# Performance work log

Measured on AMD Instinct MI355X. Metric: run time of the kernel, lower is better.

Reference implementation:

```python
import jax, jax.numpy as jnp
import numpy as np

D = 2048
B = 32768
EPS = 1e-5


def _branch_params(key, d):
    k1, k2 = jax.random.split(key)
    s1 = 1.0 / np.sqrt(d)
    return dict(
        W1=jax.random.uniform(k1, (d, d), jnp.float32, -s1, s1),
        b1=jnp.zeros((d,), jnp.float32),
        ln_g=jnp.ones((d,), jnp.float32),
        ln_b=jnp.zeros((d,), jnp.float32),
        W2=jax.random.uniform(k2, (2, d), jnp.float32, -s1, s1),
        b2=jnp.zeros((2,), jnp.float32),
    )


def setup_inputs() -> dict:
    key = jax.random.key(0)
    kx, kf, ka, kr = jax.random.split(key, 4)
    x = jax.random.normal(kx, (B, D), jnp.float32)
    inp = {"x": x}
    for name, k in (("first", kf), ("fake", ka), ("real", kr)):
        p = _branch_params(k, D)
        for pn, pv in p.items():
            inp[f"{name}_{pn}"] = pv
    return inp


def _branch(x, W1, b1, g, be, W2, b2):
    # Linear(d,d) -> LayerNorm(d) -> ReLU -> Linear(d,2); Dropout is identity at eval.
    h = x @ W1.T + b1                                   # [B, D]
    mu = jnp.mean(h, axis=-1, keepdims=True)
    var = jnp.mean(jnp.square(h - mu), axis=-1, keepdims=True)
    h = (h - mu) * jax.lax.rsqrt(var + EPS) * g + be
    h = jax.nn.relu(h)
    return h @ W2.T + b2                                # [B, 2]


def reference(x,
              first_W1, first_b1, first_ln_g, first_ln_b, first_W2, first_b2,
              fake_W1, fake_b1, fake_ln_g, fake_ln_b, fake_W2, fake_b2,
              real_W1, real_b1, real_ln_g, real_ln_b, real_W2, real_b2):
    first_logits = _branch(x, first_W1, first_b1, first_ln_g, first_ln_b, first_W2, first_b2)
    route = jnp.argmax(first_logits, axis=1)            # [B], 0 -> fake expert, else real
    fake_logits = _branch(x, fake_W1, fake_b1, fake_ln_g, fake_ln_b, fake_W2, fake_b2)
    real_logits = _branch(x, real_W1, real_b1, real_ln_g, real_ln_b, real_W2, real_b2)
    final_logits = jnp.where((route == 0)[:, None], fake_logits, real_logits)  # [B, 2]
    return final_logits
```

## Files before the change

### kernel.cpp

```cpp
#include <hip/hip_runtime.h>

#define BD 32768
#define DD 2048
#define LN_EPS 1e-5f
#define MARGIN 0.03f
#define UCAP 8192
#define IDX_CAP 33280

typedef unsigned short u16;
typedef unsigned int u32;
typedef __bf16 bf16x8 __attribute__((ext_vector_type(8)));
typedef float floatx4 __attribute__((ext_vector_type(4)));

__device__ inline u16 f2bf(float f) {
    u32 u = __builtin_bit_cast(u32, f);
    u32 r = (u + 0x7fffu + ((u >> 16) & 1u)) >> 16;
    return (u16)r;
}
__device__ inline float bf2f(u16 h) {
    return __builtin_bit_cast(float, ((u32)h) << 16);
}
__device__ inline void bf2x2(u32 p, float& lo, float& hi) {
    lo = __builtin_bit_cast(float, p << 16);
    hi = __builtin_bit_cast(float, p & 0xffff0000u);
}

__device__ inline void lds16(const void* g, void* l) {
    __builtin_amdgcn_global_load_lds(
        (const __attribute__((address_space(1))) u32*)g,
        (__attribute__((address_space(3))) u32*)l, 16, 0, 0);
}

__global__ __launch_bounds__(256) void zero_misc(int* idx_all, int* u_idx, int* ctrl) {
    int t = blockIdx.x * 256 + threadIdx.x;
    if (t < IDX_CAP) idx_all[t] = 0;
    if (t < UCAP) u_idx[t] = 0;
    if (t < 8) ctrl[t] = 0;
}

__global__ __launch_bounds__(256) void split_xhi(const float* __restrict__ in,
                                                 u16* __restrict__ hi, int n4) {
    int i = blockIdx.x * 256 + threadIdx.x;
    if (i >= n4) return;
    float4 f = ((const float4*)in)[i];
    ((ushort4*)hi)[i] = make_ushort4(f2bf(f.x), f2bf(f.y), f2bf(f.z), f2bf(f.w));
}

__global__ __launch_bounds__(256) void split_xlo(const float* __restrict__ x,
                                                 const int* __restrict__ u_idx,
                                                 const int* __restrict__ ctrl,
                                                 u16* __restrict__ xlo) {
    int u = ctrl[1]; if (u > UCAP) u = UCAP;
    int r = blockIdx.x;
    if (r >= u) return;
    int orig = u_idx[r];
    const float4* src = (const float4*)(x + (size_t)orig * DD);
    ushort4* dst = (ushort4*)(xlo + (size_t)r * DD);
    int i = threadIdx.x;
#pragma unroll
    for (int k = 0; k < 2; ++k, i += 256) {
        float4 f = src[i];
        u16 h0 = f2bf(f.x), h1 = f2bf(f.y), h2 = f2bf(f.z), h3 = f2bf(f.w);
        dst[i] = make_ushort4(f2bf(f.x - bf2f(h0)), f2bf(f.y - bf2f(h1)),
                              f2bf(f.z - bf2f(h2)), f2bf(f.w - bf2f(h3)));
    }
}

__global__ __launch_bounds__(256) void split_w3(const float* __restrict__ w0,
                                                const float* __restrict__ w1,
                                                const float* __restrict__ w2,
                                                u16* h0, u16* l0p,
                                                u16* h1, u16* l1p,
                                                u16* h2, u16* l2p) {
    int i = blockIdx.x * 256 + threadIdx.x;
    int m = blockIdx.y;
    const float* in = (m == 0) ? w0 : (m == 1) ? w1 : w2;
    u16* hi = (m == 0) ? h0 : (m == 1) ? h1 : h2;
    u16* lo = (m == 0) ? l0p : (m == 1) ? l1p : l2p;
    float4 f = ((const float4*)in)[i];
    u16 a0 = f2bf(f.x), a1 = f2bf(f.y), a2 = f2bf(f.z), a3 = f2bf(f.w);
    u16 b0 = f2bf(f.x - bf2f(a0)), b1 = f2bf(f.y - bf2f(a1));
    u16 b2 = f2bf(f.z - bf2f(a2)), b3 = f2bf(f.w - bf2f(a3));
    ((ushort4*)hi)[i] = make_ushort4(a0, a1, a2, a3);
    ((ushort4*)lo)[i] = make_ushort4(b0, b1, b2, b3);
}

template <int IDX, int DUAL>
__global__ __launch_bounds__(512, 2) void gemm256(const u16* __restrict__ A,
                                                  const u16* __restrict__ B1,
                                                  const u16* __restrict__ B2,
                                                  u16* __restrict__ C,
                                                  const int* __restrict__ ridx,
                                                  const int* __restrict__ ctrl) {
    const int nwg = (int)(gridDim.x * gridDim.y);
    const int wg0 = (int)(blockIdx.y * gridDim.x + blockIdx.x);
    const int chunk = nwg >> 3;
    const int swz = (wg0 & 7) * chunk + (wg0 >> 3);
    const size_t bm = (size_t)(swz >> 3) * 256;
    const size_t bn = (size_t)(swz & 7) * 256;

    const u16* Bp = B1;
    if (DUAL) {
        int nf_pad = ctrl[3];
        int limit = nf_pad + (BD - ctrl[2]);
        if ((int)bm >= limit) return;
        if ((int)bm >= nf_pad) Bp = B2;
    }

    __shared__ alignas(16) u16 smem[65536];
    const int tid = threadIdx.x;
    const int lane = tid & 63;
    const int wave = tid >> 6;
    const int wr = wave >> 2, wc = wave & 3;
    const int m16 = lane & 15, q4 = lane >> 4;

    const int srow = tid >> 3;
    const int kq = ((tid & 7) ^ (srow & 7)) * 8;
    const int tid8 = tid * 8;
    size_t aOff[4], bOff[4];
#pragma unroll
    for (int s = 0; s < 4; ++s) {
        int row = s * 64 + srow;
        int g = IDX ? ridx[bm + row] : (int)(bm + row);
        aOff[s] = (size_t)g * DD + kq;
        bOff[s] = (size_t)(bn + row) * DD + kq;
    }

    const int slot0 = ((q4) ^ (m16 & 7)) * 8;
    const int slot1 = ((4 + q4) ^ (m16 & 7)) * 8;
    const int aFr = (wr * 128 + m16) * 64;
    const int bFr = 16384 + (wc * 64 + m16) * 64;

    floatx4 acc[8][4] = {};

#define STAGE_TILE(DB, K0)                                              \
    lds16(A + aOff[0] + (K0), &smem[(DB) + 0 * 4096 + tid8]);           \
    lds16(A + aOff[1] + (K0), &smem[(DB) + 1 * 4096 + tid8]);           \
    lds16(A + aOff[2] + (K0), &smem[(DB) + 2 * 4096 + tid8]);           \
    lds16(A + aOff[3] + (K0), &smem[(DB) + 3 * 4096 + tid8]);           \
    lds16(Bp + bOff[0] + (K0), &smem[(DB) + 16384 + 0 * 4096 + tid8]);  \
    lds16(Bp + bOff[1] + (K0), &smem[(DB) + 16384 + 1 * 4096 + tid8]);  \
    lds16(Bp + bOff[2] + (K0), &smem[(DB) + 16384 + 2 * 4096 + tid8]);  \
    lds16(Bp + bOff[3] + (K0), &smem[(DB) + 16384 + 3 * 4096 + tid8]);

    STAGE_TILE(0, 0)

    int base = 0;
    const int NT = DD / 64;
    for (int t = 0; t < NT; ++t) {
        const int nbase = base ^ 32768;
        __builtin_amdgcn_s_barrier();
        if (t + 1 < NT) {
            STAGE_TILE(nbase, (t + 1) * 64)
            asm volatile("s_waitcnt vmcnt(8)" ::: "memory");
        } else {
            asm volatile("s_waitcnt vmcnt(0)" ::: "memory");
        }
        __builtin_amdgcn_s_barrier();
        __builtin_amdgcn_sched_barrier(0);

        bf16x8 bfr[2][4];
#pragma unroll
        for (int j = 0; j < 4; ++j) {
            bfr[0][j] = *(const bf16x8*)&smem[base + bFr + j * 1024 + slot0];
            bfr[1][j] = *(const bf16x8*)&smem[base + bFr + j * 1024 + slot1];
        }
#pragma unroll
        for (int p = 0; p < 4; ++p) {
            bf16x8 a0k0 = *(const bf16x8*)&smem[base + aFr + (2 * p) * 1024 + slot0];
            bf16x8 a0k1 = *(const bf16x8*)&smem[base + aFr + (2 * p) * 1024 + slot1];
            bf16x8 a1k0 = *(const bf16x8*)&smem[base + aFr + (2 * p + 1) * 1024 + slot0];
            bf16x8 a1k1 = *(const bf16x8*)&smem[base + aFr + (2 * p + 1) * 1024 + slot1];
            __builtin_amdgcn_s_setprio(1);
#pragma unroll
            for (int j = 0; j < 4; ++j) {
                acc[2 * p][j]     = __builtin_amdgcn_mfma_f32_16x16x32_bf16(a0k0, bfr[0][j], acc[2 * p][j], 0, 0, 0);
                acc[2 * p][j]     = __builtin_amdgcn_mfma_f32_16x16x32_bf16(a0k1, bfr[1][j], acc[2 * p][j], 0, 0, 0);
                acc[2 * p + 1][j] = __builtin_amdgcn_mfma_f32_16x16x32_bf16(a1k0, bfr[0][j], acc[2 * p + 1][j], 0, 0, 0);
                acc[2 * p + 1][j] = __builtin_amdgcn_mfma_f32_16x16x32_bf16(a1k1, bfr[1][j], acc[2 * p + 1][j], 0, 0, 0);
            }
            __builtin_amdgcn_s_setprio(0);
        }
        base = nbase;
    }
#undef STAGE_TILE

#pragma unroll
    for (int i = 0; i < 8; ++i) {
#pragma unroll
        for (int r = 0; r < 4; ++r) {
            size_t grow = bm + wr * 128 + i * 16 + q4 * 4 + r;
            u16* crow = C + grow * DD + bn + wc * 64 + m16;
#pragma unroll
            for (int j = 0; j < 4; ++j) crow[j * 16] = f2bf(acc[i][j][r]);
        }
    }
}

__global__ __launch_bounds__(256) void gemm_split(const u16* __restrict__ Ahi,
                                                  const u16* __restrict__ Alo,
                                                  const u16* __restrict__ Bhi,
                                                  const u16* __restrict__ Blo,
                                                  float* __restrict__ C,
                                                  const int* __restrict__ ridx,
                                                  const int* __restrict__ ctrl) {
    const int tid = threadIdx.x;
    const size_t bm = (size_t)blockIdx.y * 128;
    const size_t bn = (size_t)blockIdx.x * 128;

    int u = ctrl[1]; if (u > UCAP) u = UCAP;
    if ((int)bm >= u) return;

    __shared__ alignas(16) u16 smem[2 * 16384];
    const int lane = tid & 63;
    const int wave = tid >> 6;
    const int wm = (wave >> 1) * 64, wn = (wave & 1) * 64;
    const int m16 = lane & 15, q = lane >> 4;
    const int swzf = (q ^ ((m16 >> 1) & 3)) * 8;

    int aRow[2], gRow[2], kqv[2];
    size_t bOff[2];
#pragma unroll
    for (int s = 0; s < 2; ++s) {
        int e = s * 256 + tid;
        int row = e >> 2;
        int c = e & 3;
        kqv[s] = (c ^ ((row >> 1) & 3)) * 8;
        aRow[s] = ridx[bm + row];
        gRow[s] = (int)bm + row;
        bOff[s] = (size_t)(bn + row) * DD;
    }

    floatx4 acc[4][4] = {};

#define SPLIT_STAGE(DB, K0)                                                       \
    lds16(Ahi + (size_t)aRow[0] * DD + (K0) + kqv[0], &smem[(DB) + tid * 8]);     \
    lds16(Ahi + (size_t)aRow[1] * DD + (K0) + kqv[1], &smem[(DB) + 2048 + tid * 8]); \
    lds16(Bhi + bOff[0] + (K0) + kqv[0], &smem[(DB) + 4096 + tid * 8]);           \
    lds16(Bhi + bOff[1] + (K0) + kqv[1], &smem[(DB) + 6144 + tid * 8]);           \
    lds16(Alo + (size_t)gRow[0] * DD + (K0) + kqv[0], &smem[(DB) + 8192 + tid * 8]); \
    lds16(Alo + (size_t)gRow[1] * DD + (K0) + kqv[1], &smem[(DB) + 10240 + tid * 8]); \
    lds16(Blo + bOff[0] + (K0) + kqv[0], &smem[(DB) + 12288 + tid * 8]);          \
    lds16(Blo + bOff[1] + (K0) + kqv[1], &smem[(DB) + 14336 + tid * 8]);

    SPLIT_STAGE(0, 0)
    int base = 0;
    const int NTS = DD / 32;
    for (int t = 0; t < NTS; ++t) {
        const int nbase = base ^ 16384;
        __builtin_amdgcn_s_barrier();
        if (t + 1 < NTS) {
            SPLIT_STAGE(nbase, (t + 1) * 32)
            asm volatile("s_waitcnt vmcnt(8)" ::: "memory");
        } else {
            asm volatile("s_waitcnt vmcnt(0)" ::: "memory");
        }
        __builtin_amdgcn_s_barrier();
        __builtin_amdgcn_sched_barrier(0);

        bf16x8 ah[4], bh[4], al[4], bl[4];
#pragma unroll
        for (int i = 0; i < 4; ++i) {
            ah[i] = *(const bf16x8*)&smem[base + (wm + i * 16 + m16) * 32 + swzf];
            bh[i] = *(const bf16x8*)&smem[base + 4096 + (wn + i * 16 + m16) * 32 + swzf];
            al[i] = *(const bf16x8*)&smem[base + 8192 + (wm + i * 16 + m16) * 32 + swzf];
            bl[i] = *(const bf16x8*)&smem[base + 12288 + (wn + i * 16 + m16) * 32 + swzf];
        }
        __builtin_amdgcn_s_setprio(1);
#pragma unroll
        for (int i = 0; i < 4; ++i)
#pragma unroll
            for (int j = 0; j < 4; ++j) {
                acc[i][j] = __builtin_amdgcn_mfma_f32_16x16x32_bf16(ah[i], bh[j], acc[i][j], 0, 0, 0);
                acc[i][j] = __builtin_amdgcn_mfma_f32_16x16x32_bf16(ah[i], bl[j], acc[i][j], 0, 0, 0);
                acc[i][j] = __builtin_amdgcn_mfma_f32_16x16x32_bf16(al[i], bh[j], acc[i][j], 0, 0, 0);
            }
        __builtin_amdgcn_s_setprio(0);
        base = nbase;
    }
#undef SPLIT_STAGE

#pragma unroll
    for (int i = 0; i < 4; ++i)
#pragma unroll
        for (int r = 0; r < 4; ++r) {
            size_t grow = bm + wm + i * 16 + q * 4 + r;
            float* crow = C + grow * DD + bn + wn + m16;
#pragma unroll
            for (int j = 0; j < 4; ++j) crow[j * 16] = acc[i][j][r];
        }
}

__device__ inline void stage_params(float* __restrict__ sp,
                                    const float* __restrict__ b1,
                                    const float* __restrict__ g,
                                    const float* __restrict__ be,
                                    const float* __restrict__ W2, int tid) {
#pragma unroll
    for (int k = 0; k < 2; ++k) {
        int idx = (k * 256 + tid) * 4;
        *(float4*)&sp[idx]          = *(const float4*)&b1[idx];
        *(float4*)&sp[2048 + idx]   = *(const float4*)&g[idx];
        *(float4*)&sp[4096 + idx]   = *(const float4*)&be[idx];
        *(float4*)&sp[6144 + idx]   = *(const float4*)&W2[idx];
        *(float4*)&sp[8192 + idx]   = *(const float4*)&W2[2048 + idx];
    }
}

__device__ inline void ln_row(const u16* __restrict__ hr,
                              const float* __restrict__ sp,
                              int lane, float b20, float b21,
                              float& L0, float& L1) {
    const int cb = lane * 8;
    uint4 h0 = *(const uint4*)(hr + 0 * 512 + cb);
    uint4 h1 = *(const uint4*)(hr + 1 * 512 + cb);
    uint4 h2 = *(const uint4*)(hr + 2 * 512 + cb);
    uint4 h3 = *(const uint4*)(hr + 3 * 512 + cb);

    float sum = 0.f, sumsq = 0.f;
#define LN_STATS(HV, C)                                                        \
    {                                                                          \
        int col = (C) * 512 + cb;                                              \
        float4 b0 = *(const float4*)(sp + col);                                \
        float4 b4 = *(const float4*)(sp + col + 4);                            \
        float f0, f1, f2, f3, f4, f5, f6, f7;                                  \
        bf2x2(HV.x, f0, f1); bf2x2(HV.y, f2, f3);                              \
        bf2x2(HV.z, f4, f5); bf2x2(HV.w, f6, f7);                              \
        f0 += b0.x; f1 += b0.y; f2 += b0.z; f3 += b0.w;                        \
        f4 += b4.x; f5 += b4.y; f6 += b4.z; f7 += b4.w;                        \
        sum += ((f0 + f1) + (f2 + f3)) + ((f4 + f5) + (f6 + f7));              \
        sumsq += ((f0 * f0 + f1 * f1) + (f2 * f2 + f3 * f3)) +                 \
                 ((f4 * f4 + f5 * f5) + (f6 * f6 + f7 * f7));                  \
    }
    LN_STATS(h0, 0) LN_STATS(h1, 1) LN_STATS(h2, 2) LN_STATS(h3, 3)
#undef LN_STATS
#pragma unroll
    for (int off = 32; off > 0; off >>= 1) {
        sum += __shfl_xor(sum, off);
        sumsq += __shfl_xor(sumsq, off);
    }
    const float mu = sum * (1.f / 2048.f);
    const float var = sumsq * (1.f / 2048.f) - mu * mu;
    const float rstd = rsqrtf(var + LN_EPS);

    float l0 = 0.f, l1 = 0.f;
#define LN_HEAD(HV, C)                                                         \
    {                                                                          \
        int col = (C) * 512 + cb;                                              \
        float4 b0 = *(const float4*)(sp + col);                                \
        float4 b4 = *(const float4*)(sp + col + 4);                            \
        float4 g0 = *(const float4*)(sp + 2048 + col);                         \
        float4 g4 = *(const float4*)(sp + 2048 + col + 4);                     \
        float4 e0 = *(const float4*)(sp + 4096 + col);                         \
        float4 e4 = *(const float4*)(sp + 4096 + col + 4);                     \
        float4 w00 = *(const float4*)(sp + 6144 + col);                        \
        float4 w04 = *(const float4*)(sp + 6144 + col + 4);                    \
        float4 w10 = *(const float4*)(sp + 8192 + col);                        \
        float4 w14 = *(const float4*)(sp + 8192 + col + 4);                    \
        float f0, f1, f2, f3, f4, f5, f6, f7, hn;                              \
        bf2x2(HV.x, f0, f1); bf2x2(HV.y, f2, f3);                              \
        bf2x2(HV.z, f4, f5); bf2x2(HV.w, f6, f7);                              \
        hn = fmaxf(((f0 + b0.x) - mu) * rstd * g0.x + e0.x, 0.f); l0 += hn * w00.x; l1 += hn * w10.x; \
        hn = fmaxf(((f1 + b0.y) - mu) * rstd * g0.y + e0.y, 0.f); l0 += hn * w00.y; l1 += hn * w10.y; \
        hn = fmaxf(((f2 + b0.z) - mu) * rstd * g0.z + e0.z, 0.f); l0 += hn * w00.z; l1 += hn * w10.z; \
        hn = fmaxf(((f3 + b0.w) - mu) * rstd * g0.w + e0.w, 0.f); l0 += hn * w00.w; l1 += hn * w10.w; \
        hn = fmaxf(((f4 + b4.x) - mu) * rstd * g4.x + e4.x, 0.f); l0 += hn * w04.x; l1 += hn * w14.x; \
        hn = fmaxf(((f5 + b4.y) - mu) * rstd * g4.y + e4.y, 0.f); l0 += hn * w04.y; l1 += hn * w14.y; \
        hn = fmaxf(((f6 + b4.z) - mu) * rstd * g4.z + e4.z, 0.f); l0 += hn * w04.z; l1 += hn * w14.z; \
        hn = fmaxf(((f7 + b4.w) - mu) * rstd * g4.w + e4.w, 0.f); l0 += hn * w04.w; l1 += hn * w14.w; \
    }
    LN_HEAD(h0, 0) LN_HEAD(h1, 1) LN_HEAD(h2, 2) LN_HEAD(h3, 3)
#undef LN_HEAD
#pragma unroll
    for (int off = 32; off > 0; off >>= 1) {
        l0 += __shfl_xor(l0, off);
        l1 += __shfl_xor(l1, off);
    }
    L0 = l0 + b20;
    L1 = l1 + b21;
}

__device__ inline void ln_core(const float* __restrict__ hr,
                               const float* __restrict__ b1,
                               const float* __restrict__ g,
                               const float* __restrict__ be,
                               const float* __restrict__ W2,
                               const float* __restrict__ b2,
                               int lane, float& L0, float& L1) {
    float v[32];
    float sum = 0.f, sumsq = 0.f;
#pragma unroll
    for (int i = 0; i < 8; ++i) {
        int col = i * 256 + lane * 4;
        float4 t = *(const float4*)(hr + col);
        float4 bb = *(const float4*)(b1 + col);
        t.x += bb.x; t.y += bb.y; t.z += bb.z; t.w += bb.w;
        v[i * 4 + 0] = t.x; v[i * 4 + 1] = t.y; v[i * 4 + 2] = t.z; v[i * 4 + 3] = t.w;
        sum += t.x + t.y + t.z + t.w;
        sumsq += t.x * t.x + t.y * t.y + t.z * t.z + t.w * t.w;
    }
#pragma unroll
    for (int off = 32; off > 0; off >>= 1) {
        sum += __shfl_xor(sum, off);
        sumsq += __shfl_xor(sumsq, off);
    }
    const float mu = sum * (1.f / 2048.f);
    const float var = sumsq * (1.f / 2048.f) - mu * mu;
    const float rstd = rsqrtf(var + LN_EPS);

    float l0 = 0.f, l1 = 0.f;
#pragma unroll
    for (int i = 0; i < 8; ++i) {
        int col = i * 256 + lane * 4;
        float4 gg = *(const float4*)(g + col);
        float4 bbe = *(const float4*)(be + col);
        float4 w0 = *(const float4*)(W2 + col);
        float4 w1 = *(const float4*)(W2 + DD + col);
        float hn;
        hn = fmaxf((v[i * 4 + 0] - mu) * rstd * gg.x + bbe.x, 0.f); l0 += hn * w0.x; l1 += hn * w1.x;
        hn = fmaxf((v[i * 4 + 1] - mu) * rstd * gg.y + bbe.y, 0.f); l0 += hn * w0.y; l1 += hn * w1.y;
        hn = fmaxf((v[i * 4 + 2] - mu) * rstd * gg.z + bbe.z, 0.f); l0 += hn * w0.z; l1 += hn * w1.z;
        hn = fmaxf((v[i * 4 + 3] - mu) * rstd * gg.w + bbe.w, 0.f); l0 += hn * w0.w; l1 += hn * w1.w;
    }
#pragma unroll
    for (int off = 32; off > 0; off >>= 1) {
        l0 += __shfl_xor(l0, off);
        l1 += __shfl_xor(l1, off);
    }
    L0 = l0 + b2[0];
    L1 = l1 + b2[1];
}

__global__ __launch_bounds__(256) void ln_route(const u16* __restrict__ h,
                                                const float* __restrict__ b1,
                                                const float* __restrict__ g,
                                                const float* __restrict__ be,
                                                const float* __restrict__ W2,
                                                const float* __restrict__ b2,
                                                int* __restrict__ route,
                                                int* __restrict__ ctrl,
                                                int* __restrict__ u_idx) {
    __shared__ float sp[5 * 2048];
    __shared__ int blk_nf;
    const int tid = threadIdx.x;
    if (tid == 0) blk_nf = 0;
    stage_params(sp, b1, g, be, W2, tid);
    __syncthreads();
    const int wave = tid >> 6, lane = tid & 63;
    const int r = blockIdx.x * 4 + wave;
    float l0, l1;
    ln_row(h + (size_t)r * DD, sp, lane, b2[0], b2[1], l0, l1);
    if (lane == 0) {
        int rt = (l0 >= l1) ? 0 : 1;
        route[r] = rt;
        if (rt == 0) atomicAdd(&blk_nf, 1);
        if (fabsf(l0 - l1) < MARGIN) {
            int p = atomicAdd(&ctrl[1], 1);
            if (p < UCAP) u_idx[p] = r;
        }
    }
    __syncthreads();
    if (tid == 0 && blk_nf) atomicAdd(&ctrl[0], blk_nf);
}

__global__ __launch_bounds__(256) void ln_fixup(const float* __restrict__ h,
                                                const float* __restrict__ b1,
                                                const float* __restrict__ g,
                                                const float* __restrict__ be,
                                                const float* __restrict__ W2,
                                                const float* __restrict__ b2,
                                                int* __restrict__ route,
                                                int* __restrict__ ctrl,
                                                const int* __restrict__ u_idx) {
    const int wave = threadIdx.x >> 6, lane = threadIdx.x & 63;
    const int r = blockIdx.x * 4 + wave;
    int u = ctrl[1]; if (u > UCAP) u = UCAP;
    if (r >= u) return;
    const int orig = u_idx[r];
    float l0, l1;
    ln_core(h + (size_t)r * DD, b1, g, be, W2, b2, lane, l0, l1);
    if (lane == 0) {
        int rt = (l0 >= l1) ? 0 : 1;
        int old = route[orig];
        if (rt != old) {
            atomicAdd(&ctrl[0], rt == 0 ? 1 : -1);
            route[orig] = rt;
        }
    }
}

__global__ void init_ctrl(int* ctrl) {
    int nf = ctrl[0];
    ctrl[2] = nf;
    ctrl[3] = (nf + 255) & ~255;
    ctrl[4] = 0;
    ctrl[5] = ctrl[3];
}

__global__ __launch_bounds__(256) void compact(const int* __restrict__ route,
                                               int* __restrict__ ctrl,
                                               int* __restrict__ idx_all) {
    const int row = blockIdx.x * 256 + threadIdx.x;
    const int lane = threadIdx.x & 63;
    const bool isf = (route[row] == 0);
    unsigned long long m = __ballot(isf);
    int nfw = __popcll(m);
    int baseF = 0, baseR = 0;
    if (lane == 0) {
        baseF = atomicAdd(&ctrl[4], nfw);
        baseR = atomicAdd(&ctrl[5], 64 - nfw);
    }
    baseF = __shfl(baseF, 0);
    baseR = __shfl(baseR, 0);
    unsigned long long lt = (lane == 0) ? 0ull : ((~0ull) >> (64 - lane));
    int pre = __popcll(m & lt);
    int pos = isf ? (baseF + pre) : (baseR + (lane - pre));
    idx_all[pos] = row;
}

__global__ __launch_bounds__(256) void ln_final(const u16* __restrict__ h,
                                                const float* __restrict__ b1f, const float* __restrict__ gf,
                                                const float* __restrict__ bef, const float* __restrict__ W2f,
                                                const float* __restrict__ b2f,
                                                const float* __restrict__ b1r, const float* __restrict__ gr,
                                                const float* __restrict__ ber, const float* __restrict__ W2r,
                                                const float* __restrict__ b2r,
                                                const int* __restrict__ ctrl,
                                                const int* __restrict__ idx_all,
                                                float* __restrict__ out) {
    const int nf = ctrl[2], nf_pad = ctrl[3];
    const int limit = nf_pad + (BD - nf);
    const int base = blockIdx.x * 4;
    bool fake;
    if (base < nf) fake = true;
    else if (base >= nf_pad && base < limit) fake = false;
    else return;

    __shared__ float sp[5 * 2048];
    const int tid = threadIdx.x;
    stage_params(sp, fake ? b1f : b1r, fake ? gf : gr, fake ? bef : ber,
                 fake ? W2f : W2r, tid);
    __syncthreads();
    const int wave = tid >> 6, lane = tid & 63;
    const int r = base + wave;
    if (fake ? (r < nf) : (r < limit)) {
        const float* b2 = fake ? b2f : b2r;
        float l0, l1;
        ln_row(h + (size_t)r * DD, sp, lane, b2[0], b2[1], l0, l1);
        if (lane == 0) {
            int orig = idx_all[r];
            out[(size_t)orig * 2 + 0] = l0;
            out[(size_t)orig * 2 + 1] = l1;
        }
    }
}

extern "C" void kernel_launch(void* const* d_in, const int* in_sizes, int n_in,
                              void* d_out, int out_size, void* d_ws, size_t ws_size,
                              hipStream_t stream) {
    const float* x = (const float*)d_in[0];
    const float* W1[3] = {(const float*)d_in[1], (const float*)d_in[7], (const float*)d_in[13]};
    const float* b1[3] = {(const float*)d_in[2], (const float*)d_in[8], (const float*)d_in[14]};
    const float* lg[3] = {(const float*)d_in[3], (const float*)d_in[9], (const float*)d_in[15]};
    const float* lb[3] = {(const float*)d_in[4], (const float*)d_in[10], (const float*)d_in[16]};
    const float* W2[3] = {(const float*)d_in[5], (const float*)d_in[11], (const float*)d_in[17]};
    const float* b2[3] = {(const float*)d_in[6], (const float*)d_in[12], (const float*)d_in[18]};

    char* ws = (char*)d_ws;
    size_t off = 0;
    u16* x_hi = (u16*)(ws + off); off += (size_t)BD * DD * 2;
    u16* x_lo = (u16*)(ws + off); off += (size_t)UCAP * DD * 2;
    u16* w_hi[3];
    u16* w_lo[3];
    for (int i = 0; i < 3; ++i) { w_hi[i] = (u16*)(ws + off); off += (size_t)DD * DD * 2; }
    for (int i = 0; i < 3; ++i) { w_lo[i] = (u16*)(ws + off); off += (size_t)DD * DD * 2; }
    u16* h16 = (u16*)(ws + off); off += (size_t)IDX_CAP * DD * 2;
    float* hfix = (float*)(ws + off); off += (size_t)UCAP * DD * 4;
    int* route = (int*)(ws + off); off += (size_t)BD * 4;
    int* idx_all = (int*)(ws + off); off += (size_t)IDX_CAP * 4;
    int* u_idx = (int*)(ws + off); off += (size_t)UCAP * 4;
    int* ctrl = (int*)(ws + off); off += 64;

    zero_misc<<<(IDX_CAP + 255) / 256, 256, 0, stream>>>(idx_all, u_idx, ctrl);

    split_xhi<<<(BD * DD / 4) / 256, 256, 0, stream>>>(x, x_hi, BD * DD / 4);
    split_w3<<<dim3((DD * DD / 4) / 256, 3), 256, 0, stream>>>(
        W1[0], W1[1], W1[2], w_hi[0], w_lo[0], w_hi[1], w_lo[1], w_hi[2], w_lo[2]);

    gemm256<0, 0><<<dim3(DD / 256, BD / 256), 512, 0, stream>>>(
        x_hi, w_hi[0], nullptr, h16, nullptr, nullptr);
    ln_route<<<BD / 4, 256, 0, stream>>>(h16, b1[0], lg[0], lb[0], W2[0], b2[0],
                                         route, ctrl, u_idx);

    split_xlo<<<UCAP, 256, 0, stream>>>(x, u_idx, ctrl, x_lo);
    gemm_split<<<dim3(DD / 128, UCAP / 128), 256, 0, stream>>>(
        x_hi, x_lo, w_hi[0], w_lo[0], hfix, u_idx, ctrl);
    ln_fixup<<<UCAP / 4, 256, 0, stream>>>(hfix, b1[0], lg[0], lb[0], W2[0], b2[0],
                                           route, ctrl, u_idx);

    init_ctrl<<<1, 1, 0, stream>>>(ctrl);
    compact<<<BD / 256, 256, 0, stream>>>(route, ctrl, idx_all);

    gemm256<1, 1><<<dim3(DD / 256, BD / 256 + 1), 512, 0, stream>>>(
        x_hi, w_hi[1], w_hi[2], h16, idx_all, ctrl);

    ln_final<<<IDX_CAP / 4, 256, 0, stream>>>(
        h16, b1[1], lg[1], lb[1], W2[1], b2[1],
        b1[2], lg[2], lb[2], W2[2], b2[2],
        ctrl, idx_all, (float*)d_out);
}
```

Before: 1.240 ms.

## Interleave next-tile global loads with MFMA phases and batch LN rows per block

The gemm256 main loop no longer issues all eight next-tile LDS-direct loads up front behind a barrier. It spreads them in pairs across the four MFMA sub-phases, with a mid-iteration wait and barrier, and peels the last iteration out of the loop. The aim is to hide global-load latency behind compute and remove one barrier per K step, at the cost of fine-grained vmcnt bookkeeping that must stay correct. Separately, ln_route and ln_final now process four rows per wave (16 per block), which cuts the per-block parameter staging into shared memory by a factor of four.

```diff
diff --git a/kernel.cpp b/kernel.cpp
--- a/kernel.cpp
+++ b/kernel.cpp
@@ -133,31 +133,23 @@
 
     floatx4 acc[8][4] = {};
 
-#define STAGE_TILE(DB, K0)                                              \
-    lds16(A + aOff[0] + (K0), &smem[(DB) + 0 * 4096 + tid8]);           \
-    lds16(A + aOff[1] + (K0), &smem[(DB) + 1 * 4096 + tid8]);           \
-    lds16(A + aOff[2] + (K0), &smem[(DB) + 2 * 4096 + tid8]);           \
-    lds16(A + aOff[3] + (K0), &smem[(DB) + 3 * 4096 + tid8]);           \
-    lds16(Bp + bOff[0] + (K0), &smem[(DB) + 16384 + 0 * 4096 + tid8]);  \
-    lds16(Bp + bOff[1] + (K0), &smem[(DB) + 16384 + 1 * 4096 + tid8]);  \
-    lds16(Bp + bOff[2] + (K0), &smem[(DB) + 16384 + 2 * 4096 + tid8]);  \
-    lds16(Bp + bOff[3] + (K0), &smem[(DB) + 16384 + 3 * 4096 + tid8]);
-
-    STAGE_TILE(0, 0)
+    lds16(Bp + bOff[0], &smem[16384 + 0 * 4096 + tid8]);
+    lds16(Bp + bOff[1], &smem[16384 + 1 * 4096 + tid8]);
+    lds16(A + aOff[0], &smem[0 * 4096 + tid8]);
+    lds16(A + aOff[2], &smem[2 * 4096 + tid8]);
+    lds16(Bp + bOff[2], &smem[16384 + 2 * 4096 + tid8]);
+    lds16(Bp + bOff[3], &smem[16384 + 3 * 4096 + tid8]);
+    lds16(A + aOff[1], &smem[1 * 4096 + tid8]);
+    lds16(A + aOff[3], &smem[3 * 4096 + tid8]);
+    asm volatile("s_waitcnt vmcnt(2)" ::: "memory");
+    __builtin_amdgcn_s_barrier();
+    __builtin_amdgcn_sched_barrier(0);
 
     int base = 0;
     const int NT = DD / 64;
-    for (int t = 0; t < NT; ++t) {
+    for (int t = 0; t < NT - 1; ++t) {
         const int nbase = base ^ 32768;
-        __builtin_amdgcn_s_barrier();
-        if (t + 1 < NT) {
-            STAGE_TILE(nbase, (t + 1) * 64)
-            asm volatile("s_waitcnt vmcnt(8)" ::: "memory");
-        } else {
-            asm volatile("s_waitcnt vmcnt(0)" ::: "memory");
-        }
-        __builtin_amdgcn_s_barrier();
-        __builtin_amdgcn_sched_barrier(0);
+        const int k0n = (t + 1) * 64;
 
         bf16x8 bfr[2][4];
 #pragma unroll
@@ -165,8 +157,27 @@
             bfr[0][j] = *(const bf16x8*)&smem[base + bFr + j * 1024 + slot0];
             bfr[1][j] = *(const bf16x8*)&smem[base + bFr + j * 1024 + slot1];
         }
+
 #pragma unroll
         for (int p = 0; p < 4; ++p) {
+            if (p == 0) {
+                lds16(Bp + bOff[0] + k0n, &smem[nbase + 16384 + 0 * 4096 + tid8]);
+                lds16(Bp + bOff[1] + k0n, &smem[nbase + 16384 + 1 * 4096 + tid8]);
+            } else if (p == 1) {
+                lds16(A + aOff[0] + k0n, &smem[nbase + 0 * 4096 + tid8]);
+                lds16(A + aOff[2] + k0n, &smem[nbase + 2 * 4096 + tid8]);
+            } else if (p == 2) {
+                lds16(Bp + bOff[2] + k0n, &smem[nbase + 16384 + 2 * 4096 + tid8]);
+                lds16(Bp + bOff[3] + k0n, &smem[nbase + 16384 + 3 * 4096 + tid8]);
+            } else {
+                lds16(A + aOff[1] + k0n, &smem[nbase + 1 * 4096 + tid8]);
+                lds16(A + aOff[3] + k0n, &smem[nbase + 3 * 4096 + tid8]);
+            }
+            if (p == 2) {
+                asm volatile("s_waitcnt vmcnt(6)" ::: "memory");
+                __builtin_amdgcn_s_barrier();
+                __builtin_amdgcn_sched_barrier(0);
+            }
             bf16x8 a0k0 = *(const bf16x8*)&smem[base + aFr + (2 * p) * 1024 + slot0];
             bf16x8 a0k1 = *(const bf16x8*)&smem[base + aFr + (2 * p) * 1024 + slot1];
             bf16x8 a1k0 = *(const bf16x8*)&smem[base + aFr + (2 * p + 1) * 1024 + slot0];
@@ -181,9 +192,42 @@
             }
             __builtin_amdgcn_s_setprio(0);
         }
+
+        asm volatile("s_waitcnt vmcnt(2)" ::: "memory");
+        __builtin_amdgcn_s_barrier();
+        __builtin_amdgcn_sched_barrier(0);
         base = nbase;
     }
-#undef STAGE_TILE
+
+    {
+        bf16x8 bfr[2][4];
+#pragma unroll
+        for (int j = 0; j < 4; ++j) {
+            bfr[0][j] = *(const bf16x8*)&smem[base + bFr + j * 1024 + slot0];
+            bfr[1][j] = *(const bf16x8*)&smem[base + bFr + j * 1024 + slot1];
+        }
+#pragma unroll
+        for (int p = 0; p < 4; ++p) {
+            if (p == 2) {
+                asm volatile("s_waitcnt vmcnt(0)" ::: "memory");
+                __builtin_amdgcn_s_barrier();
+                __builtin_amdgcn_sched_barrier(0);
+            }
+            bf16x8 a0k0 = *(const bf16x8*)&smem[base + aFr + (2 * p) * 1024 + slot0];
+            bf16x8 a0k1 = *(const bf16x8*)&smem[base + aFr + (2 * p) * 1024 + slot1];
+            bf16x8 a1k0 = *(const bf16x8*)&smem[base + aFr + (2 * p + 1) * 1024 + slot0];
+            bf16x8 a1k1 = *(const bf16x8*)&smem[base + aFr + (2 * p + 1) * 1024 + slot1];
+            __builtin_amdgcn_s_setprio(1);
+#pragma unroll
+            for (int j = 0; j < 4; ++j) {
+                acc[2 * p][j]     = __builtin_amdgcn_mfma_f32_16x16x32_bf16(a0k0, bfr[0][j], acc[2 * p][j], 0, 0, 0);
+                acc[2 * p][j]     = __builtin_amdgcn_mfma_f32_16x16x32_bf16(a0k1, bfr[1][j], acc[2 * p][j], 0, 0, 0);
+                acc[2 * p + 1][j] = __builtin_amdgcn_mfma_f32_16x16x32_bf16(a1k0, bfr[0][j], acc[2 * p + 1][j], 0, 0, 0);
+                acc[2 * p + 1][j] = __builtin_amdgcn_mfma_f32_16x16x32_bf16(a1k1, bfr[1][j], acc[2 * p + 1][j], 0, 0, 0);
+            }
+            __builtin_amdgcn_s_setprio(0);
+        }
+    }
 
 #pragma unroll
     for (int i = 0; i < 8; ++i) {
@@ -447,18 +491,25 @@
     stage_params(sp, b1, g, be, W2, tid);
     __syncthreads();
     const int wave = tid >> 6, lane = tid & 63;
-    const int r = blockIdx.x * 4 + wave;
-    float l0, l1;
-    ln_row(h + (size_t)r * DD, sp, lane, b2[0], b2[1], l0, l1);
-    if (lane == 0) {
-        int rt = (l0 >= l1) ? 0 : 1;
-        route[r] = rt;
-        if (rt == 0) atomicAdd(&blk_nf, 1);
-        if (fabsf(l0 - l1) < MARGIN) {
-            int p = atomicAdd(&ctrl[1], 1);
-            if (p < UCAP) u_idx[p] = r;
-        }
-    }
+    const float b20 = b2[0], b21 = b2[1];
+    const int rbase = blockIdx.x * 16 + wave * 4;
+    int local_nf = 0;
+#pragma unroll
+    for (int k = 0; k < 4; ++k) {
+        const int r = rbase + k;
+        float l0, l1;
+        ln_row(h + (size_t)r * DD, sp, lane, b20, b21, l0, l1);
+        if (lane == 0) {
+            int rt = (l0 >= l1) ? 0 : 1;
+            route[r] = rt;
+            local_nf += (rt == 0);
+            if (fabsf(l0 - l1) < MARGIN) {
+                int p = atomicAdd(&ctrl[1], 1);
+                if (p < UCAP) u_idx[p] = r;
+            }
+        }
+    }
+    if (lane == 0 && local_nf) atomicAdd(&blk_nf, local_nf);
     __syncthreads();
     if (tid == 0 && blk_nf) atomicAdd(&ctrl[0], blk_nf);
 }
@@ -530,11 +581,12 @@
                                                 float* __restrict__ out) {
     const int nf = ctrl[2], nf_pad = ctrl[3];
     const int limit = nf_pad + (BD - nf);
-    const int base = blockIdx.x * 4;
+    const int base = blockIdx.x * 16;
     bool fake;
     if (base < nf) fake = true;
     else if (base >= nf_pad && base < limit) fake = false;
     else return;
+    const int bound = fake ? nf : limit;
 
     __shared__ float sp[5 * 2048];
     const int tid = threadIdx.x;
@@ -542,11 +594,15 @@
                  fake ? W2f : W2r, tid);
     __syncthreads();
     const int wave = tid >> 6, lane = tid & 63;
-    const int r = base + wave;
-    if (fake ? (r < nf) : (r < limit)) {
-        const float* b2 = fake ? b2f : b2r;
+    const float* b2 = fake ? b2f : b2r;
+    const float b20 = b2[0], b21 = b2[1];
+    const int rbase = base + wave * 4;
+#pragma unroll
+    for (int k = 0; k < 4; ++k) {
+        const int r = rbase + k;
+        if (r >= bound) break;
         float l0, l1;
-        ln_row(h + (size_t)r * DD, sp, lane, b2[0], b2[1], l0, l1);
+        ln_row(h + (size_t)r * DD, sp, lane, b20, b21, l0, l1);
         if (lane == 0) {
             int orig = idx_all[r];
             out[(size_t)orig * 2 + 0] = l0;
@@ -589,8 +645,8 @@
 
     gemm256<0, 0><<<dim3(DD / 256, BD / 256), 512, 0, stream>>>(
         x_hi, w_hi[0], nullptr, h16, nullptr, nullptr);
-    ln_route<<<BD / 4, 256, 0, stream>>>(h16, b1[0], lg[0], lb[0], W2[0], b2[0],
-                                         route, ctrl, u_idx);
+    ln_route<<<BD / 16, 256, 0, stream>>>(h16, b1[0], lg[0], lb[0], W2[0], b2[0],
+                                          route, ctrl, u_idx);
 
     split_xlo<<<UCAP, 256, 0, stream>>>(x, u_idx, ctrl, x_lo);
     gemm_split<<<dim3(DD / 128, UCAP / 128), 256, 0, stream>>>(
@@ -604,7 +660,7 @@
     gemm256<1, 1><<<dim3(DD / 256, BD / 256 + 1), 512, 0, stream>>>(
         x_hi, w_hi[1], w_hi[2], h16, idx_all, ctrl);
 
-    ln_final<<<IDX_CAP / 4, 256, 0, stream>>>(
+    ln_final<<<IDX_CAP / 16, 256, 0, stream>>>(
         h16, b1[1], lg[1], lb[1], W2[1], b2[1],
         b1[2], lg[2], lb[2], W2[2], b2[2],
         ctrl, idx_all, (float*)d_out);
```

Result: faster. 1.098 ms (-11.4%).
